# Kernel optimization log

Hardware: AMD Instinct MI355X
Metric: run time of the kernel (lower is better)

The kernel has to match this reference:

```python
import jax, jax.numpy as jnp
import numpy as np

EPS = 1e-7
LABEL_SMOOTHING = 0.1

def label2onehot(labels, pad_value):
    # labels: [B,T] int -> multi-hot [B, pad_value] with pad column dropped and index 0 zeroed
    oh = jax.nn.one_hot(labels, pad_value + 1, dtype=jnp.float32)  # [B,T,P+1]
    oh = oh.max(axis=1)[:, :-1]                                    # [B,P]
    return oh.at[:, 0].set(0.0)

def mask_from_eos(ids, eos_value):
    # mult_before=False variant: mask[:,0]=1, mask[:,t]=prod_{j=1..t}(ids[:,j]!=eos)
    ne = (ids != eos_value).astype(jnp.float32)
    ne = ne.at[:, 0].set(1.0)
    return jnp.cumprod(ne, axis=1)

def bce(p, t):
    p = jnp.clip(p, EPS, 1.0 - EPS)
    return -(t * jnp.log(p) + (1.0 - t) * jnp.log1p(-p))

def setup_inputs():
    key = jax.random.key(0)
    k1, k2, k3 = jax.random.split(key, 3)
    B, T, P = 4096, 20, 1488  # batch, max ingredients, ingredient vocab (= pad_value)
    return {
        "ingr_logits": jax.random.normal(k1, (B, T, P), dtype=jnp.float32),
        "target_ingrs": jax.random.randint(k2, (B, T), 0, P + 1, dtype=jnp.int32),
        "ingr_ids": jax.random.randint(k3, (B, T), 0, P + 1, dtype=jnp.int32),
        "pad_value": P,
    }

def reference(ingr_logits, target_ingrs, ingr_ids, pad_value):
    probs = jax.nn.softmax(ingr_logits, axis=-1)            # [B,T,P]
    eos = probs[:, :, 0]                                    # [B,T]

    t_oh = label2onehot(target_ingrs, pad_value)            # [B,P]
    denom = jnp.float32(t_oh.shape[-1])
    t_oh_smooth = jnp.where(t_oh == 0, LABEL_SMOOTHING / denom, 1.0 - LABEL_SMOOTHING)

    target_eos = ((target_ingrs == 0) ^ (target_ingrs == pad_value)).astype(jnp.float32)
    eos_pos = (target_ingrs == 0).astype(jnp.float32)
    eos_head = ((target_ingrs != pad_value) & (target_ingrs != 0)).astype(jnp.float32)

    mask = mask_from_eos(target_ingrs, 0)                   # [B,T]
    ingr_probs = (probs * mask[:, :, None]).max(axis=1)     # [B,P] permutation-invariant max
    ingr_ids_m = jnp.where(mask == 0, pad_value, ingr_ids)

    ingr_loss = bce(ingr_probs, t_oh_smooth).mean()

    card_penalty = (jnp.abs((ingr_probs * t_oh).sum(axis=1))
                    - t_oh.sum(axis=1)
                    + jnp.abs((ingr_probs * (1.0 - t_oh)).sum(axis=1)))

    eos_l = bce(eos, target_eos)                            # [B,T]
    mult = 0.5
    eos_loss = (mult * (eos_l * eos_pos).sum(axis=1) / (eos_pos.sum(axis=1) + 1e-6)
                + mult * (eos_l * eos_head).sum(axis=1) / (eos_head.sum(axis=1) + 1e-6))

    pred_oh = label2onehot(ingr_ids_m, pad_value)           # [B,P]
    num = (pred_oh * t_oh).sum(axis=1)
    den = (pred_oh + t_oh - pred_oh * t_oh).sum(axis=1) + 1e-6
    iou = 1.0 - num / den                                   # softIoU loss per sample

    return (ingr_loss, card_penalty, eos_loss, iou)
```

## Files before the change

### kernel.cpp

```cpp
#include <hip/hip_runtime.h>
#include <math.h>

#define BATCH 4096
#define TSEQ  20
#define PDIM  1488
#define PADV  1488
#define NSLOT 372
#define EPSF  1e-7f

typedef float f32x4 __attribute__((ext_vector_type(4)));

__device__ __forceinline__ f32x4 ntload(const f32x4* p) {
    return __builtin_nontemporal_load(p);
}

__device__ __forceinline__ float bce_f(float p, float t) {
    p = fminf(fmaxf(p, EPSF), 1.0f - EPSF);
    return -(t * __logf(p) + (1.0f - t) * log1pf(-p));
}

__device__ __forceinline__ float wave_sum(float v) {
    #pragma unroll
    for (int m = 1; m < 64; m <<= 1) v += __shfl_xor(v, m, 64);
    return v;
}

__global__ __launch_bounds__(256) void icm_main_kernel(
    const float* __restrict__ logits,
    const int*   __restrict__ target,
    const int*   __restrict__ ids,
    float*       __restrict__ out,
    float*       __restrict__ ws)
{
    const int lane = threadIdx.x & 63;
    const int wid  = threadIdx.x >> 6;
    const int b    = blockIdx.x * 4 + wid;

    const bool v5 = (lane < 52);

    int tvr = (lane < TSEQ) ? target[b * TSEQ + lane] : PADV;
    int idr = (lane < TSEQ) ? ids[b * TSEQ + lane]    : PADV;

    unsigned rowmask = 0, tohm = 0, predm = 0;
    int ok = 1;
    #pragma unroll
    for (int j = 0; j < TSEQ; ++j) {
        int v = __shfl(tvr, j, 64);
        if (j > 0 && v == 0) ok = 0;
        if (ok) rowmask |= 1u << j;
        if (v >= 1 && v < PDIM) {
            int s = v >> 2;
            if ((s & 63) == lane) tohm |= 1u << (((s >> 6) << 2) | (v & 3));
        }
        int iv = __shfl(idr, j, 64);
        int mv = ok ? iv : PADV;
        if (mv >= 1 && mv < PDIM) {
            int s = mv >> 2;
            if ((s & 63) == lane) predm |= 1u << (((s >> 6) << 2) | (mv & 3));
        }
    }

    const f32x4* base = (const f32x4*)(logits + (size_t)b * TSEQ * PDIM);
    const int slot5 = v5 ? (lane + 320) : 371;

    f32x4 run[6];
    #pragma unroll
    for (int k = 0; k < 6; ++k) run[k] = (f32x4)(0.f);

    float acc_pos = 0.f, acc_head = 0.f, n_pos = 0.f, n_head = 0.f;

    f32x4 A[6], B[6];

    #pragma unroll
    for (int k = 0; k < 5; ++k) A[k] = ntload(base + lane + 64 * k);
    A[5] = ntload(base + slot5);

    #pragma unroll
    for (int t = 0; t < TSEQ; t += 2) {
        {
            const f32x4* p = base + (size_t)(t + 1) * NSLOT;
            #pragma unroll
            for (int k = 0; k < 5; ++k) B[k] = ntload(p + lane + 64 * k);
            B[5] = ntload(p + slot5);
        }

        {
            float ssum = 0.f;
            #pragma unroll
            for (int k = 0; k < 6; ++k) {
                bool val = (k < 5) || v5;
                f32x4 v = A[k], e;
                e.x = val ? __expf(v.x) : 0.f;
                e.y = val ? __expf(v.y) : 0.f;
                e.z = val ? __expf(v.z) : 0.f;
                e.w = val ? __expf(v.w) : 0.f;
                A[k] = e;
                ssum += (e.x + e.y) + (e.z + e.w);
            }
            ssum = wave_sum(ssum);
            float rinv = 1.0f / ssum;
            if ((rowmask >> t) & 1) {
                #pragma unroll
                for (int k = 0; k < 6; ++k) {
                    run[k].x = fmaxf(run[k].x, A[k].x * rinv);
                    run[k].y = fmaxf(run[k].y, A[k].y * rinv);
                    run[k].z = fmaxf(run[k].z, A[k].z * rinv);
                    run[k].w = fmaxf(run[k].w, A[k].w * rinv);
                }
            }
            float eosp = A[0].x * rinv;
            int   tvt  = __shfl(tvr, t, 64);
            float te   = (tvt == 0 || tvt == PADV) ? 1.f : 0.f;
            float el   = bce_f(eosp, te);
            float ep   = (tvt == 0) ? 1.f : 0.f;
            float eh   = (tvt != 0 && tvt != PADV) ? 1.f : 0.f;
            acc_pos += el * ep;  n_pos += ep;
            acc_head += el * eh; n_head += eh;
        }

        if (t + 2 < TSEQ) {
            const f32x4* p = base + (size_t)(t + 2) * NSLOT;
            #pragma unroll
            for (int k = 0; k < 5; ++k) A[k] = ntload(p + lane + 64 * k);
            A[5] = ntload(p + slot5);
        }

        {
            float ssum = 0.f;
            #pragma unroll
            for (int k = 0; k < 6; ++k) {
                bool val = (k < 5) || v5;
                f32x4 v = B[k], e;
                e.x = val ? __expf(v.x) : 0.f;
                e.y = val ? __expf(v.y) : 0.f;
                e.z = val ? __expf(v.z) : 0.f;
                e.w = val ? __expf(v.w) : 0.f;
                B[k] = e;
                ssum += (e.x + e.y) + (e.z + e.w);
            }
            ssum = wave_sum(ssum);
            float rinv = 1.0f / ssum;
            if ((rowmask >> (t + 1)) & 1) {
                #pragma unroll
                for (int k = 0; k < 6; ++k) {
                    run[k].x = fmaxf(run[k].x, B[k].x * rinv);
                    run[k].y = fmaxf(run[k].y, B[k].y * rinv);
                    run[k].z = fmaxf(run[k].z, B[k].z * rinv);
                    run[k].w = fmaxf(run[k].w, B[k].w * rinv);
                }
            }
            float eosp = B[0].x * rinv;
            int   tvt  = __shfl(tvr, t + 1, 64);
            float te   = (tvt == 0 || tvt == PADV) ? 1.f : 0.f;
            float el   = bce_f(eosp, te);
            float ep   = (tvt == 0) ? 1.f : 0.f;
            float eh   = (tvt != 0 && tvt != PADV) ? 1.f : 0.f;
            acc_pos += el * ep;  n_pos += eh * 0.f + ep;
            acc_head += el * eh; n_head += eh;
        }
    }

    float bce_sum = 0.f, s1 = 0.f, s2 = 0.f, ntc = 0.f, inter = 0.f, uni = 0.f;
    #pragma unroll
    for (int k = 0; k < 6; ++k) {
        if (k == 5 && !v5) break;
        float rp[4] = {run[k].x, run[k].y, run[k].z, run[k].w};
        #pragma unroll
        for (int j = 0; j < 4; ++j) {
            float toh = ((tohm  >> (k * 4 + j)) & 1) ? 1.f : 0.f;
            float pr  = ((predm >> (k * 4 + j)) & 1) ? 1.f : 0.f;
            float ts  = (toh > 0.f) ? 0.9f : (0.1f / 1488.0f);
            bce_sum += bce_f(rp[j], ts);
            s1    += rp[j] * toh;
            s2    += rp[j] * (1.f - toh);
            ntc   += toh;
            inter += pr * toh;
            uni   += pr + toh - pr * toh;
        }
    }

    bce_sum = wave_sum(bce_sum);
    s1      = wave_sum(s1);
    s2      = wave_sum(s2);
    ntc     = wave_sum(ntc);
    inter   = wave_sum(inter);
    uni     = wave_sum(uni);

    if (lane == 0) {
        ws[b] = bce_sum;
        out[1 + b]             = fabsf(s1) - ntc + fabsf(s2);
        out[1 + BATCH + b]     = 0.5f * acc_pos / (n_pos + 1e-6f)
                               + 0.5f * acc_head / (n_head + 1e-6f);
        out[1 + 2 * BATCH + b] = 1.0f - inter / (uni + 1e-6f);
    }
}

__global__ __launch_bounds__(256) void icm_reduce_kernel(
    const float* __restrict__ ws, float* __restrict__ out)
{
    int tid = threadIdx.x;
    float v = 0.f;
    for (int i = tid; i < BATCH; i += 256) v += ws[i];
    #pragma unroll
    for (int m = 1; m < 64; m <<= 1) v += __shfl_xor(v, m, 64);
    __shared__ float buf[4];
    int lane = tid & 63, wid = tid >> 6;
    if (lane == 0) buf[wid] = v;
    __syncthreads();
    if (tid == 0) {
        float t = (buf[0] + buf[1]) + (buf[2] + buf[3]);
        out[0] = t / ((float)BATCH * (float)PDIM);
    }
}

extern "C" void kernel_launch(void* const* d_in, const int* in_sizes, int n_in,
                              void* d_out, int out_size, void* d_ws, size_t ws_size,
                              hipStream_t stream) {
    const float* logits = (const float*)d_in[0];
    const int*   target = (const int*)d_in[1];
    const int*   ids    = (const int*)d_in[2];

    float* out = (float*)d_out;
    float* ws  = (float*)d_ws;

    hipLaunchKernelGGL(icm_main_kernel, dim3(BATCH / 4), dim3(256), 0, stream,
                       logits, target, ids, out, ws);
    hipLaunchKernelGGL(icm_reduce_kernel, dim3(1), dim3(256), 0, stream,
                       ws, out);
}
```

Before: 633.6 us.

## Split each sample's time steps across four waves with shared-memory max merge

Each sample now gets a full 256-thread block instead of one wave. Each of the four waves handles five interleaved time rows, and the per-wave running maxima and EOS partial sums are merged through shared memory by wave 0. This shortens each wave's serial chain of row loads and softmaxes, giving more parallelism and memory-level concurrency. The cost is LDS traffic, a block barrier, three idle waves during the final reduction, and four times as many blocks.

```diff
diff --git a/kernel.cpp b/kernel.cpp
--- a/kernel.cpp
+++ b/kernel.cpp
@@ -7,6 +7,8 @@
 #define PADV  1488
 #define NSLOT 372
 #define EPSF  1e-7f
+#define NW    4
+#define RPW   5
 
 typedef float f32x4 __attribute__((ext_vector_type(4)));
 
@@ -34,9 +36,11 @@
 {
     const int lane = threadIdx.x & 63;
     const int wid  = threadIdx.x >> 6;
-    const int b    = blockIdx.x * 4 + wid;
-
-    const bool v5 = (lane < 52);
+    const int b    = blockIdx.x;
+    const bool v5  = (lane < 52);
+
+    __shared__ f32x4 s_run[NW - 1][NSLOT];
+    __shared__ float s_eos[NW][4];
 
     int tvr = (lane < TSEQ) ? target[b * TSEQ + lane] : PADV;
     int idr = (lane < TSEQ) ? ids[b * TSEQ + lane]    : PADV;
@@ -60,105 +64,99 @@
         }
     }
 
-    const f32x4* base = (const f32x4*)(logits + (size_t)b * TSEQ * PDIM);
-    const int slot5 = v5 ? (lane + 320) : 371;
+    const f32x4* base  = (const f32x4*)(logits + (size_t)b * TSEQ * PDIM);
+    const int    slot5 = v5 ? (lane + 320) : 371;
 
     f32x4 run[6];
     #pragma unroll
     for (int k = 0; k < 6; ++k) run[k] = (f32x4)(0.f);
-
     float acc_pos = 0.f, acc_head = 0.f, n_pos = 0.f, n_head = 0.f;
 
     f32x4 A[6], B[6];
 
-    #pragma unroll
-    for (int k = 0; k < 5; ++k) A[k] = ntload(base + lane + 64 * k);
-    A[5] = ntload(base + slot5);
-
-    #pragma unroll
-    for (int t = 0; t < TSEQ; t += 2) {
-        {
-            const f32x4* p = base + (size_t)(t + 1) * NSLOT;
-            #pragma unroll
-            for (int k = 0; k < 5; ++k) B[k] = ntload(p + lane + 64 * k);
-            B[5] = ntload(p + slot5);
-        }
-
-        {
-            float ssum = 0.f;
+    auto loadrow = [&](f32x4 (&buf)[6], int t) {
+        const f32x4* p = base + (size_t)t * NSLOT;
+        #pragma unroll
+        for (int k = 0; k < 5; ++k) buf[k] = ntload(p + lane + 64 * k);
+        buf[5] = ntload(p + slot5);
+    };
+
+    auto process = [&](f32x4 (&buf)[6], int t) {
+        float ssum = 0.f;
+        #pragma unroll
+        for (int k = 0; k < 6; ++k) {
+            bool val = (k < 5) || v5;
+            f32x4 v = buf[k], e;
+            e.x = val ? __expf(v.x) : 0.f;
+            e.y = val ? __expf(v.y) : 0.f;
+            e.z = val ? __expf(v.z) : 0.f;
+            e.w = val ? __expf(v.w) : 0.f;
+            buf[k] = e;
+            ssum += (e.x + e.y) + (e.z + e.w);
+        }
+        ssum = wave_sum(ssum);
+        float rinv = 1.0f / ssum;
+        if ((rowmask >> t) & 1) {
             #pragma unroll
             for (int k = 0; k < 6; ++k) {
-                bool val = (k < 5) || v5;
-                f32x4 v = A[k], e;
-                e.x = val ? __expf(v.x) : 0.f;
-                e.y = val ? __expf(v.y) : 0.f;
-                e.z = val ? __expf(v.z) : 0.f;
-                e.w = val ? __expf(v.w) : 0.f;
-                A[k] = e;
-                ssum += (e.x + e.y) + (e.z + e.w);
+                run[k].x = fmaxf(run[k].x, buf[k].x * rinv);
+                run[k].y = fmaxf(run[k].y, buf[k].y * rinv);
+                run[k].z = fmaxf(run[k].z, buf[k].z * rinv);
+                run[k].w = fmaxf(run[k].w, buf[k].w * rinv);
             }
-            ssum = wave_sum(ssum);
-            float rinv = 1.0f / ssum;
-            if ((rowmask >> t) & 1) {
-                #pragma unroll
-                for (int k = 0; k < 6; ++k) {
-                    run[k].x = fmaxf(run[k].x, A[k].x * rinv);
-                    run[k].y = fmaxf(run[k].y, A[k].y * rinv);
-                    run[k].z = fmaxf(run[k].z, A[k].z * rinv);
-                    run[k].w = fmaxf(run[k].w, A[k].w * rinv);
-                }
-            }
-            float eosp = A[0].x * rinv;
-            int   tvt  = __shfl(tvr, t, 64);
-            float te   = (tvt == 0 || tvt == PADV) ? 1.f : 0.f;
-            float el   = bce_f(eosp, te);
-            float ep   = (tvt == 0) ? 1.f : 0.f;
-            float eh   = (tvt != 0 && tvt != PADV) ? 1.f : 0.f;
-            acc_pos += el * ep;  n_pos += ep;
-            acc_head += el * eh; n_head += eh;
-        }
-
-        if (t + 2 < TSEQ) {
-            const f32x4* p = base + (size_t)(t + 2) * NSLOT;
-            #pragma unroll
-            for (int k = 0; k < 5; ++k) A[k] = ntload(p + lane + 64 * k);
-            A[5] = ntload(p + slot5);
-        }
-
-        {
-            float ssum = 0.f;
-            #pragma unroll
-            for (int k = 0; k < 6; ++k) {
-                bool val = (k < 5) || v5;
-                f32x4 v = B[k], e;
-                e.x = val ? __expf(v.x) : 0.f;
-                e.y = val ? __expf(v.y) : 0.f;
-                e.z = val ? __expf(v.z) : 0.f;
-                e.w = val ? __expf(v.w) : 0.f;
-                B[k] = e;
-                ssum += (e.x + e.y) + (e.z + e.w);
-            }
-            ssum = wave_sum(ssum);
-            float rinv = 1.0f / ssum;
-            if ((rowmask >> (t + 1)) & 1) {
-                #pragma unroll
-                for (int k = 0; k < 6; ++k) {
-                    run[k].x = fmaxf(run[k].x, B[k].x * rinv);
-                    run[k].y = fmaxf(run[k].y, B[k].y * rinv);
-                    run[k].z = fmaxf(run[k].z, B[k].z * rinv);
-                    run[k].w = fmaxf(run[k].w, B[k].w * rinv);
-                }
-            }
-            float eosp = B[0].x * rinv;
-            int   tvt  = __shfl(tvr, t + 1, 64);
-            float te   = (tvt == 0 || tvt == PADV) ? 1.f : 0.f;
-            float el   = bce_f(eosp, te);
-            float ep   = (tvt == 0) ? 1.f : 0.f;
-            float eh   = (tvt != 0 && tvt != PADV) ? 1.f : 0.f;
-            acc_pos += el * ep;  n_pos += eh * 0.f + ep;
-            acc_head += el * eh; n_head += eh;
-        }
-    }
+        }
+        float eosp = buf[0].x * rinv;
+        int   tvt  = __shfl(tvr, t, 64);
+        float te   = (tvt == 0 || tvt == PADV) ? 1.f : 0.f;
+        float el   = bce_f(eosp, te);
+        float ep   = (tvt == 0) ? 1.f : 0.f;
+        float eh   = (tvt != 0 && tvt != PADV) ? 1.f : 0.f;
+        acc_pos  += el * ep;  n_pos  += ep;
+        acc_head += el * eh;  n_head += eh;
+    };
+
+    const int t0 = wid;
+    loadrow(A, t0);
+    loadrow(B, t0 + 4);
+    process(A, t0);
+    loadrow(A, t0 + 8);
+    process(B, t0 + 4);
+    loadrow(B, t0 + 12);
+    process(A, t0 + 8);
+    loadrow(A, t0 + 16);
+    process(B, t0 + 12);
+    process(A, t0 + 16);
+
+    if (wid > 0) {
+        #pragma unroll
+        for (int k = 0; k < 5; ++k) s_run[wid - 1][lane + 64 * k] = run[k];
+        if (v5) s_run[wid - 1][lane + 320] = run[5];
+    }
+    if (lane == 0) {
+        s_eos[wid][0] = acc_pos;  s_eos[wid][1] = n_pos;
+        s_eos[wid][2] = acc_head; s_eos[wid][3] = n_head;
+    }
+    __syncthreads();
+    if (wid != 0) return;
+
+    #pragma unroll
+    for (int k = 0; k < 6; ++k) {
+        if (k == 5 && !v5) break;
+        const int slot = (k < 5) ? (lane + 64 * k) : (lane + 320);
+        #pragma unroll
+        for (int w = 0; w < NW - 1; ++w) {
+            f32x4 o = s_run[w][slot];
+            run[k].x = fmaxf(run[k].x, o.x);
+            run[k].y = fmaxf(run[k].y, o.y);
+            run[k].z = fmaxf(run[k].z, o.z);
+            run[k].w = fmaxf(run[k].w, o.w);
+        }
+    }
+
+    float ap = s_eos[0][0] + s_eos[1][0] + s_eos[2][0] + s_eos[3][0];
+    float np = s_eos[0][1] + s_eos[1][1] + s_eos[2][1] + s_eos[3][1];
+    float ah = s_eos[0][2] + s_eos[1][2] + s_eos[2][2] + s_eos[3][2];
+    float nh = s_eos[0][3] + s_eos[1][3] + s_eos[2][3] + s_eos[3][3];
 
     float bce_sum = 0.f, s1 = 0.f, s2 = 0.f, ntc = 0.f, inter = 0.f, uni = 0.f;
     #pragma unroll
@@ -169,8 +167,8 @@
         for (int j = 0; j < 4; ++j) {
             float toh = ((tohm  >> (k * 4 + j)) & 1) ? 1.f : 0.f;
             float pr  = ((predm >> (k * 4 + j)) & 1) ? 1.f : 0.f;
-            float ts  = (toh > 0.f) ? 0.9f : (0.1f / 1488.0f);
-            bce_sum += bce_f(rp[j], ts);
+            float tsm = (toh > 0.f) ? 0.9f : (0.1f / 1488.0f);
+            bce_sum += bce_f(rp[j], tsm);
             s1    += rp[j] * toh;
             s2    += rp[j] * (1.f - toh);
             ntc   += toh;
@@ -189,8 +187,8 @@
     if (lane == 0) {
         ws[b] = bce_sum;
         out[1 + b]             = fabsf(s1) - ntc + fabsf(s2);
-        out[1 + BATCH + b]     = 0.5f * acc_pos / (n_pos + 1e-6f)
-                               + 0.5f * acc_head / (n_head + 1e-6f);
+        out[1 + BATCH + b]     = 0.5f * ap / (np + 1e-6f)
+                               + 0.5f * ah / (nh + 1e-6f);
         out[1 + 2 * BATCH + b] = 1.0f - inter / (uni + 1e-6f);
     }
 }
@@ -223,7 +221,7 @@
     float* out = (float*)d_out;
     float* ws  = (float*)d_ws;
 
-    hipLaunchKernelGGL(icm_main_kernel, dim3(BATCH / 4), dim3(256), 0, stream,
+    hipLaunchKernelGGL(icm_main_kernel, dim3(BATCH), dim3(256), 0, stream,
                        logits, target, ids, out, ws);
     hipLaunchKernelGGL(icm_reduce_kernel, dim3(1), dim3(256), 0, stream,
                        ws, out);
```

Result: faster. 613.4 us (-3.2%).
